# Kernel tuning notes

Hardware: AMD Instinct MI355X
Metric: run time of the kernel (lower is better)

The kernel has to match this reference:

```python
import jax, jax.numpy as jnp
import numpy as np

EMBED_DIM = 1024
NUM_HEADS = 16
HEAD_DIM = EMBED_DIM // NUM_HEADS
B, S = 2, 2048


def setup_inputs() -> dict:
    key = jax.random.key(0)
    ks = jax.random.split(key, 9)
    scale = 1.0 / np.sqrt(EMBED_DIM)
    return {
        "x": jax.random.normal(ks[0], (B, S, EMBED_DIM), dtype=jnp.float32),
        "Wq": jax.random.normal(ks[1], (EMBED_DIM, EMBED_DIM), dtype=jnp.float32) * scale,
        "bq": jnp.zeros((EMBED_DIM,), dtype=jnp.float32),
        "Wk": jax.random.normal(ks[2], (EMBED_DIM, EMBED_DIM), dtype=jnp.float32) * scale,
        "bk": jnp.zeros((EMBED_DIM,), dtype=jnp.float32),
        "Wv": jax.random.normal(ks[3], (EMBED_DIM, EMBED_DIM), dtype=jnp.float32) * scale,
        "bv": jnp.zeros((EMBED_DIM,), dtype=jnp.float32),
        "Wo": jax.random.normal(ks[4], (EMBED_DIM, EMBED_DIM), dtype=jnp.float32) * scale,
        "bo": jnp.zeros((EMBED_DIM,), dtype=jnp.float32),
    }


def _split_heads(t):
    # [B, S, E] -> [B, H, S, Dh]
    b, s, _ = t.shape
    return t.reshape(b, s, NUM_HEADS, HEAD_DIM).transpose(0, 2, 1, 3)


def reference(x, Wq, bq, Wk, bk, Wv, bv, Wo, bo):
    q = _split_heads(x @ Wq + bq)
    k = _split_heads(x @ Wk + bk)
    v = _split_heads(x @ Wv + bv)
    scale = jnp.sqrt(jnp.asarray(HEAD_DIM, dtype=x.dtype))
    scores = jnp.einsum("bhqd,bhkd->bhqk", q, k) / scale
    attn = jax.nn.softmax(scores, axis=-1)
    out = jnp.einsum("bhqk,bhkd->bhqd", attn, v)  # [B,H,S,Dh]
    out = out.transpose(0, 2, 1, 3).reshape(x.shape[0], x.shape[1], EMBED_DIM)
    return out @ Wo + bo
```

## Files before the change

### kernel.cpp

```cpp
#include <hip/hip_runtime.h>
#include <math.h>
#include <stdint.h>

typedef __bf16 bf16;
typedef __bf16 bf16x4 __attribute__((ext_vector_type(4)));
typedef __bf16 bf16x8 __attribute__((ext_vector_type(8)));
typedef float f32x4 __attribute__((ext_vector_type(4)));
typedef float f32x16 __attribute__((ext_vector_type(16)));

constexpr int E = 1024;
constexpr int S = 2048;
constexpr int H = 16;


__device__ __forceinline__ void gload16(const void* g, void* l) {
  __builtin_amdgcn_global_load_lds(
      (__attribute__((address_space(1))) void*)(uintptr_t)g,
      (__attribute__((address_space(3))) void*)(uint32_t)(uintptr_t)l, 16, 0, 0);
}

__device__ __forceinline__ f32x4 mfma16(bf16x8 a, bf16x8 b, f32x4 c) {
  return __builtin_amdgcn_mfma_f32_16x16x32_bf16(a, b, c, 0, 0, 0);
}
__device__ __forceinline__ f32x16 mfma32(bf16x8 a, bf16x8 b, f32x16 c) {
  return __builtin_amdgcn_mfma_f32_32x32x16_bf16(a, b, c, 0, 0, 0);
}

__global__ __launch_bounds__(256) void cast_x(const float* __restrict__ x,
                                              bf16* __restrict__ o) {
  const size_t i = ((size_t)blockIdx.x * 256 + threadIdx.x) * 8;
  const float4 a = *(const float4*)(x + i);
  const float4 b = *(const float4*)(x + i + 4);
  bf16x8 r;
  r[0] = (bf16)a.x; r[1] = (bf16)a.y; r[2] = (bf16)a.z; r[3] = (bf16)a.w;
  r[4] = (bf16)b.x; r[5] = (bf16)b.y; r[6] = (bf16)b.z; r[7] = (bf16)b.w;
  *(bf16x8*)(o + i) = r;
}

__global__ __launch_bounds__(256) void transpose_cast_w(
    const float* __restrict__ W0, const float* __restrict__ W1,
    const float* __restrict__ W2, const float* __restrict__ W3,
    bf16* __restrict__ T0, bf16* __restrict__ T1, bf16* __restrict__ T2,
    bf16* __restrict__ T3) {
  const float* W;
  bf16* T;
  switch (blockIdx.z) {
    case 0: W = W0; T = T0; break;
    case 1: W = W1; T = T1; break;
    case 2: W = W2; T = T2; break;
    default: W = W3; T = T3; break;
  }
  __shared__ float t[64][65];
  const int k0 = blockIdx.y * 64, n0 = blockIdx.x * 64;
  const int tr = threadIdx.x >> 4;
  const int tc = (threadIdx.x & 15) * 4;
#pragma unroll
  for (int u = 0; u < 4; ++u) {
    const float4 v = *(const float4*)(W + (size_t)(k0 + tr + u * 16) * E + n0 + tc);
    t[tr + u * 16][tc + 0] = v.x;
    t[tr + u * 16][tc + 1] = v.y;
    t[tr + u * 16][tc + 2] = v.z;
    t[tr + u * 16][tc + 3] = v.w;
  }
  __syncthreads();
#pragma unroll
  for (int u = 0; u < 4; ++u) {
    const int n = tr + u * 16;
    bf16x4 o;
#pragma unroll
    for (int i = 0; i < 4; ++i) o[i] = (bf16)t[tc + i][n];
    *(bf16x4*)(T + (size_t)(n0 + n) * E + k0 + tc) = o;
  }
}

__global__ __launch_bounds__(256) void gemm_qkv(const bf16* __restrict__ A,
                                                const bf16* __restrict__ Wt,
                                                const float* __restrict__ bq,
                                                const float* __restrict__ bk,
                                                const float* __restrict__ bv,
                                                bf16* __restrict__ qo,
                                                bf16* __restrict__ ko,
                                                bf16* __restrict__ vo) {
  __shared__ __attribute__((aligned(16))) bf16 Asm[128 * 32];
  __shared__ __attribute__((aligned(16))) bf16 Bsm[128 * 32];
  const int z = blockIdx.z;
  const bf16* Bt = Wt + (size_t)z * E * E;
  const float* bias = (z == 0) ? bq : (z == 1) ? bk : bv;
  const int tid = threadIdx.x;
  const int w = tid >> 6, lane = tid & 63, quad = lane >> 4, ln = lane & 15;
  const int bm = blockIdx.y * 128, bn = blockIdx.x * 128;
  const int wr = w >> 1, wc = w & 1;
  const int srow = w * 32 + (lane >> 2);
  const int scol = (lane & 3) * 8;
  const bf16* Ag = A + (size_t)(bm + srow) * E + scol;
  const bf16* Bg = Bt + (size_t)(bn + srow) * E + scol;
  f32x4 acc[4][4] = {};

  for (int k0 = 0; k0 < E; k0 += 32) {
    gload16(Ag + k0, &Asm[(w * 32) * 32]);
    gload16(Ag + k0 + (size_t)16 * E, &Asm[(w * 32 + 16) * 32]);
    gload16(Bg + k0, &Bsm[(w * 32) * 32]);
    gload16(Bg + k0 + (size_t)16 * E, &Bsm[(w * 32 + 16) * 32]);
    __syncthreads();
    bf16x8 af[4], bfr[4];
#pragma unroll
    for (int t = 0; t < 4; ++t) {
      af[t] = *(const bf16x8*)&Asm[(wr * 64 + t * 16 + ln) * 32 + quad * 8];
      bfr[t] = *(const bf16x8*)&Bsm[(wc * 64 + t * 16 + ln) * 32 + quad * 8];
    }
#pragma unroll
    for (int rt = 0; rt < 4; ++rt)
#pragma unroll
      for (int ct = 0; ct < 4; ++ct)
        acc[rt][ct] = mfma16(af[rt], bfr[ct], acc[rt][ct]);
    __syncthreads();
  }

  const float scl = (z == 0) ? 0.125f : 1.0f;
  const int hglob = (bn + wc * 64) >> 6;
  float bvv[4];
#pragma unroll
  for (int ct = 0; ct < 4; ++ct) bvv[ct] = bias[bn + wc * 64 + ct * 16 + ln];

#pragma unroll
  for (int rt = 0; rt < 4; ++rt) {
    const int row0 = bm + wr * 64 + rt * 16 + quad * 4;
    const int bb = row0 >> 11;
    const int rl = row0 & 2047;
    const size_t hb = (size_t)(bb * 16 + hglob) * 131072;
#pragma unroll
    for (int ct = 0; ct < 4; ++ct) {
      if (z == 2) {
        const int mt = ct >> 1, ln32 = ((ct & 1) << 4) | ln;
        const int tau = rl >> 6, hfv = (rl >> 3) & 1, j0 = rl & 7;
        bf16x4 p;
#pragma unroll
        for (int r = 0; r < 4; ++r) p[r] = (bf16)(acc[rt][ct][r] + bvv[ct]);
        *(bf16x4*)&vo[hb + (size_t)((tau * 8 + mt * 4 + rt) * 512 +
                                    hfv * 256 + ln32 * 8 + j0)] = p;
      } else {
        bf16* o = (z == 0) ? qo : ko;
        const int t = rl >> 5, ln0 = rl & 31;
        const size_t base =
            hb + (size_t)((t * 4 + ct) * 512 + (ln >> 3) * 256 + (ln & 7));
#pragma unroll
        for (int r = 0; r < 4; ++r)
          o[base + (ln0 + r) * 8] = (bf16)((acc[rt][ct][r] + bvv[ct]) * scl);
      }
    }
  }
}

__global__ __launch_bounds__(256) void gemm_wo(const bf16* __restrict__ A,
                                               const bf16* __restrict__ Bt,
                                               const float* __restrict__ bias,
                                               float* __restrict__ C) {
  __shared__ __attribute__((aligned(16))) bf16 Asm[64 * 32];
  __shared__ __attribute__((aligned(16))) bf16 Bsm[128 * 32];
  const int tid = threadIdx.x;
  const int w = tid >> 6, lane = tid & 63, quad = lane >> 4, ln = lane & 15;
  const int bm = blockIdx.y * 64, bn = blockIdx.x * 128;
  const int wr = w >> 1, wc = w & 1;
  const int sr = lane >> 2, sc = (lane & 3) * 8;
  const bf16* Ag = A + (size_t)(bm + w * 16 + sr) * E + sc;
  const bf16* Bg = Bt + (size_t)(bn + w * 32 + sr) * E + sc;
  f32x4 acc[2][4] = {};

  for (int k0 = 0; k0 < E; k0 += 32) {
    gload16(Ag + k0, &Asm[(w * 16) * 32]);
    gload16(Bg + k0, &Bsm[(w * 32) * 32]);
    gload16(Bg + k0 + (size_t)16 * E, &Bsm[(w * 32 + 16) * 32]);
    __syncthreads();
    bf16x8 af[2], bfr[4];
#pragma unroll
    for (int t = 0; t < 2; ++t)
      af[t] = *(const bf16x8*)&Asm[(wr * 32 + t * 16 + ln) * 32 + quad * 8];
#pragma unroll
    for (int t = 0; t < 4; ++t)
      bfr[t] = *(const bf16x8*)&Bsm[(wc * 64 + t * 16 + ln) * 32 + quad * 8];
#pragma unroll
    for (int rt = 0; rt < 2; ++rt)
#pragma unroll
      for (int ct = 0; ct < 4; ++ct)
        acc[rt][ct] = mfma16(af[rt], bfr[ct], acc[rt][ct]);
    __syncthreads();
  }

  float bvv[4];
#pragma unroll
  for (int ct = 0; ct < 4; ++ct) bvv[ct] = bias[bn + wc * 64 + ct * 16 + ln];
#pragma unroll
  for (int rt = 0; rt < 2; ++rt) {
    const int row0 = bm + wr * 32 + rt * 16 + quad * 4;
#pragma unroll
    for (int ct = 0; ct < 4; ++ct) {
      const int c = bn + wc * 64 + ct * 16 + ln;
#pragma unroll
      for (int r = 0; r < 4; ++r)
        C[(size_t)(row0 + r) * E + c] = acc[rt][ct][r] + bvv[ct];
    }
  }
}

__global__ __launch_bounds__(64) void attn_mfma(const bf16* __restrict__ Qf,
                                                const bf16* __restrict__ Kf,
                                                const bf16* __restrict__ Vf,
                                                bf16* __restrict__ Og) {
  __shared__ __attribute__((aligned(16))) bf16 Pl[32][74];
  const int lane = threadIdx.x;
  const int ln = lane & 31, hf = lane >> 5;
  const int tq = blockIdx.x, h = blockIdx.y, b = blockIdx.z;
  const int bh = b * H + h;
  const size_t fb = (size_t)bh * 131072;

  bf16x8 qf[4];
  {
    const bf16* qb = Qf + fb + (size_t)tq * 2048 + lane * 8;
#pragma unroll
    for (int c = 0; c < 4; ++c) qf[c] = *(const bf16x8*)(qb + c * 512);
  }

  const bf16* Kb = Kf + fb + lane * 8;
  const bf16* Vb = Vf + fb + lane * 8;

  float lpart = 0.f;
  f32x16 oacc[2] = {};

  for (int kt2 = 0; kt2 < S / 32; kt2 += 2) {
    f32x16 st[2];
#pragma unroll
    for (int mt = 0; mt < 2; ++mt) {
      const bf16* kb2 = Kb + (size_t)(kt2 + mt) * 2048;
      f32x16 zz = {};
#pragma unroll
      for (int c = 0; c < 4; ++c)
        zz = mfma32(*(const bf16x8*)(kb2 + c * 512), qf[c], zz);
      st[mt] = zz;
    }

    bf16x8 va[2][4];
    {
      const bf16* vb2 = Vb + (size_t)(kt2 >> 1) * 4096;
#pragma unroll
      for (int mt = 0; mt < 2; ++mt)
#pragma unroll
        for (int c = 0; c < 4; ++c)
          va[mt][c] = *(const bf16x8*)(vb2 + (mt * 4 + c) * 512);
    }

#pragma unroll
    for (int mt = 0; mt < 2; ++mt) {
#pragma unroll
      for (int g = 0; g < 4; ++g) {
        bf16x4 pk;
#pragma unroll
        for (int j = 0; j < 4; ++j) {
          const float p = __expf(st[mt][g * 4 + j]);
          lpart += p;
          pk[j] = (bf16)p;
        }
        *(bf16x4*)&Pl[ln][mt * 32 + g * 8 + hf * 4] = pk;
      }
    }
    asm volatile("s_waitcnt lgkmcnt(0)" ::: "memory");

    bf16x8 pb[4];
#pragma unroll
    for (int c = 0; c < 4; ++c)
      pb[c] = *(const bf16x8*)&Pl[ln][c * 16 + hf * 8];
#pragma unroll
    for (int mt = 0; mt < 2; ++mt)
#pragma unroll
      for (int c = 0; c < 4; ++c)
        oacc[mt] = mfma32(va[mt][c], pb[c], oacc[mt]);
  }

  lpart += __shfl_xor(lpart, 32);
  const float inv = 1.0f / lpart;

  bf16* orow = Og + ((size_t)b * S + (size_t)tq * 32 + ln) * E + h * 64;
#pragma unroll
  for (int mt = 0; mt < 2; ++mt) {
#pragma unroll
    for (int g = 0; g < 4; ++g) {
      bf16x4 o;
#pragma unroll
      for (int j = 0; j < 4; ++j) o[j] = (bf16)(oacc[mt][g * 4 + j] * inv);
      *(bf16x4*)&orow[mt * 32 + g * 8 + hf * 4] = o;
    }
  }
}

extern "C" void kernel_launch(void* const* d_in, const int* in_sizes, int n_in,
                              void* d_out, int out_size, void* d_ws, size_t ws_size,
                              hipStream_t stream) {
  const float* x = (const float*)d_in[0];
  const float* Wq = (const float*)d_in[1];
  const float* bq = (const float*)d_in[2];
  const float* Wk = (const float*)d_in[3];
  const float* bk = (const float*)d_in[4];
  const float* Wv = (const float*)d_in[5];
  const float* bv = (const float*)d_in[6];
  const float* Wo = (const float*)d_in[7];
  const float* bo = (const float*)d_in[8];

  const size_t ME = (size_t)4096 * 1024;
  const size_t WE = (size_t)1024 * 1024;
  bf16* xb = (bf16*)d_ws;
  bf16* wqt = xb + ME;
  bf16* wkt = wqt + WE;
  bf16* wvt = wkt + WE;
  bf16* wot = wvt + WE;
  bf16* qb = wot + WE;
  bf16* kb = qb + ME;
  bf16* vt = kb + ME;
  bf16* ab = vt + ME;

  cast_x<<<2048, 256, 0, stream>>>(x, xb);
  transpose_cast_w<<<dim3(16, 16, 4), 256, 0, stream>>>(Wq, Wk, Wv, Wo, wqt, wkt,
                                                        wvt, wot);
  gemm_qkv<<<dim3(8, 32, 3), 256, 0, stream>>>(xb, wqt, bq, bk, bv, qb, kb, vt);
  attn_mfma<<<dim3(S / 32, H, 2), 64, 0, stream>>>(qb, kb, vt, ab);
  gemm_wo<<<dim3(8, 64), 256, 0, stream>>>(ab, wot, bo, (float*)d_out);
}
```

Baseline: 204.2 us.

## Split attention keys across waves and merge partial accumulators in LDS

Attention blocks grow from one wave to four: two query tiles, each with its key range split in half across two waves. Each wave computes a partial unnormalized output and row sum. Waves with ki==1 write theirs to shared memory, and the ki==0 waves add them, normalize and store. The aim is more waves in flight and shorter per-wave serial loops, which should help latency hiding. In exchange it adds LDS traffic, a block barrier and extra LDS use. The merge is valid only because the kernel never subtracts a running max, so the partial sums combine directly.

Result: no change. 203.0 us (-0.6%).

```diff
diff --git a/kernel.cpp b/kernel.cpp
--- a/kernel.cpp
+++ b/kernel.cpp
@@ -202,16 +202,19 @@
   }
 }
 
-__global__ __launch_bounds__(64) void attn_mfma(const bf16* __restrict__ Qf,
-                                                const bf16* __restrict__ Kf,
-                                                const bf16* __restrict__ Vf,
-                                                bf16* __restrict__ Og) {
-  __shared__ __attribute__((aligned(16))) bf16 Pl[32][74];
-  const int lane = threadIdx.x;
+__global__ __launch_bounds__(256, 4) void attn_mfma(const bf16* __restrict__ Qf,
+                                                    const bf16* __restrict__ Kf,
+                                                    const bf16* __restrict__ Vf,
+                                                    bf16* __restrict__ Og) {
+  __shared__ __attribute__((aligned(16))) bf16 Pl[4][32][74];
+  __shared__ float Cb[2][32][64];
+  __shared__ float Lb[2][64];
+  const int tid = threadIdx.x;
+  const int lane = tid & 63, w = tid >> 6;
+  const int qi = w & 1, ki = w >> 1;
   const int ln = lane & 31, hf = lane >> 5;
-  const int tq = blockIdx.x, h = blockIdx.y, b = blockIdx.z;
-  const int bh = b * H + h;
-  const size_t fb = (size_t)bh * 131072;
+  const int tq = blockIdx.x * 2 + qi, h = blockIdx.y, b = blockIdx.z;
+  const size_t fb = (size_t)(b * H + h) * 131072;
 
   bf16x8 qf[4];
   {
@@ -226,7 +229,8 @@
   float lpart = 0.f;
   f32x16 oacc[2] = {};
 
-  for (int kt2 = 0; kt2 < S / 32; kt2 += 2) {
+  const int kt2lo = ki * (S / 64);
+  for (int kt2 = kt2lo; kt2 < kt2lo + S / 64; kt2 += 2) {
     f32x16 st[2];
 #pragma unroll
     for (int mt = 0; mt < 2; ++mt) {
@@ -259,7 +263,7 @@
           lpart += p;
           pk[j] = (bf16)p;
         }
-        *(bf16x4*)&Pl[ln][mt * 32 + g * 8 + hf * 4] = pk;
+        *(bf16x4*)&Pl[w][ln][mt * 32 + g * 8 + hf * 4] = pk;
       }
     }
     asm volatile("s_waitcnt lgkmcnt(0)" ::: "memory");
@@ -267,7 +271,7 @@
     bf16x8 pb[4];
 #pragma unroll
     for (int c = 0; c < 4; ++c)
-      pb[c] = *(const bf16x8*)&Pl[ln][c * 16 + hf * 8];
+      pb[c] = *(const bf16x8*)&Pl[w][ln][c * 16 + hf * 8];
 #pragma unroll
     for (int mt = 0; mt < 2; ++mt)
 #pragma unroll
@@ -275,18 +279,34 @@
         oacc[mt] = mfma32(va[mt][c], pb[c], oacc[mt]);
   }
 
-  lpart += __shfl_xor(lpart, 32);
-  const float inv = 1.0f / lpart;
-
-  bf16* orow = Og + ((size_t)b * S + (size_t)tq * 32 + ln) * E + h * 64;
-#pragma unroll
-  for (int mt = 0; mt < 2; ++mt) {
-#pragma unroll
-    for (int g = 0; g < 4; ++g) {
-      bf16x4 o;
-#pragma unroll
-      for (int j = 0; j < 4; ++j) o[j] = (bf16)(oacc[mt][g * 4 + j] * inv);
-      *(bf16x4*)&orow[mt * 32 + g * 8 + hf * 4] = o;
+  if (ki == 1) {
+#pragma unroll
+    for (int mt = 0; mt < 2; ++mt)
+#pragma unroll
+      for (int i = 0; i < 16; ++i) Cb[qi][mt * 16 + i][lane] = oacc[mt][i];
+    Lb[qi][lane] = lpart;
+  }
+  __syncthreads();
+  if (ki == 0) {
+#pragma unroll
+    for (int mt = 0; mt < 2; ++mt)
+#pragma unroll
+      for (int i = 0; i < 16; ++i) oacc[mt][i] += Cb[qi][mt * 16 + i][lane];
+    lpart += Lb[qi][lane];
+
+    lpart += __shfl_xor(lpart, 32);
+    const float inv = 1.0f / lpart;
+
+    bf16* orow = Og + ((size_t)b * S + (size_t)tq * 32 + ln) * E + h * 64;
+#pragma unroll
+    for (int mt = 0; mt < 2; ++mt) {
+#pragma unroll
+      for (int g = 0; g < 4; ++g) {
+        bf16x4 o;
+#pragma unroll
+        for (int j = 0; j < 4; ++j) o[j] = (bf16)(oacc[mt][g * 4 + j] * inv);
+        *(bf16x4*)&orow[mt * 32 + g * 8 + hf * 4] = o;
+      }
     }
   }
 }
@@ -320,6 +340,6 @@
   transpose_cast_w<<<dim3(16, 16, 4), 256, 0, stream>>>(Wq, Wk, Wv, Wo, wqt, wkt,
                                                         wvt, wot);
   gemm_qkv<<<dim3(8, 32, 3), 256, 0, stream>>>(xb, wqt, bq, bk, bv, qb, kb, vt);
-  attn_mfma<<<dim3(S / 32, H, 2), 64, 0, stream>>>(qb, kb, vt, ab);
+  attn_mfma<<<dim3(S / 64, H, 2), 256, 0, stream>>>(qb, kb, vt, ab);
   gemm_wo<<<dim3(8, 64), 256, 0, stream>>>(ab, wot, bo, (float*)d_out);
 }
```

## Share K/V tiles in LDS across query waves and split keys between wave groups

Applied to the files above, without the earlier changes.

The attention kernel becomes a 512-thread block of 8 waves. Four query tiles share K/V tiles that are loaded into LDS with global_load_lds, instead of each 64-thread block reading K/V straight from global memory. The key range is split between two wave groups, and their partial outputs and row sums are combined through LDS at the end. This aims to cut redundant global K/V traffic and raise reuse, at the cost of block-level barriers every iteration, no double-buffering, and an extra combine step.

New measurement: 191.5 us. 1.07x faster.

```diff
diff --git a/kernel.cpp b/kernel.cpp
--- a/kernel.cpp
+++ b/kernel.cpp
@@ -24,6 +24,9 @@
 }
 __device__ __forceinline__ f32x16 mfma32(bf16x8 a, bf16x8 b, f32x16 c) {
   return __builtin_amdgcn_mfma_f32_32x32x16_bf16(a, b, c, 0, 0, 0);
+}
+__device__ __forceinline__ void lgkm0() {
+  asm volatile("s_waitcnt lgkmcnt(0)" ::: "memory");
 }
 
 __global__ __launch_bounds__(256) void cast_x(const float* __restrict__ x,
@@ -202,16 +205,21 @@
   }
 }
 
-__global__ __launch_bounds__(64) void attn_mfma(const bf16* __restrict__ Qf,
-                                                const bf16* __restrict__ Kf,
-                                                const bf16* __restrict__ Vf,
-                                                bf16* __restrict__ Og) {
-  __shared__ __attribute__((aligned(16))) bf16 Pl[32][74];
-  const int lane = threadIdx.x;
-  const int ln = lane & 31, hf = lane >> 5;
-  const int tq = blockIdx.x, h = blockIdx.y, b = blockIdx.z;
-  const int bh = b * H + h;
-  const size_t fb = (size_t)bh * 131072;
+__global__ __launch_bounds__(512, 4) void attn_mfma(const bf16* __restrict__ Qf,
+                                                    const bf16* __restrict__ Kf,
+                                                    const bf16* __restrict__ Vf,
+                                                    bf16* __restrict__ Og) {
+  __shared__ __attribute__((aligned(16))) char smem[49152];
+  bf16* KsB = (bf16*)smem;
+  bf16* VsB = (bf16*)(smem + 16384);
+  bf16* PlB = (bf16*)(smem + 32768);
+
+  const int tid = threadIdx.x;
+  const int w = tid >> 6, lane = tid & 63, ln = lane & 31, hf = lane >> 5;
+  const int qi = w & 3, ki = w >> 2;
+  const int tq = blockIdx.x * 4 + qi;
+  const int h = blockIdx.y, b = blockIdx.z;
+  const size_t fb = (size_t)(b * H + h) * 131072;
 
   bf16x8 qf[4];
   {
@@ -220,73 +228,95 @@
     for (int c = 0; c < 4; ++c) qf[c] = *(const bf16x8*)(qb + c * 512);
   }
 
-  const bf16* Kb = Kf + fb + lane * 8;
-  const bf16* Vb = Vf + fb + lane * 8;
+  bf16* Ks = KsB + ki * 4096;
+  bf16* Vs = VsB + ki * 4096;
+  bf16* Pw = PlB + w * 1024;
+
+  const bf16* Ksrc = Kf + fb + qi * 1024 + lane * 8;
+  const bf16* Vsrc = Vf + fb + qi * 1024 + lane * 8;
+  bf16* Kdst = Ks + qi * 1024;
+  bf16* Vdst = Vs + qi * 1024;
 
   float lpart = 0.f;
   f32x16 oacc[2] = {};
 
-  for (int kt2 = 0; kt2 < S / 32; kt2 += 2) {
-    f32x16 st[2];
+  for (int i = 0; i < 16; ++i) {
+    const size_t toff = (size_t)(ki * 16 + i) * 4096;
+    gload16(Ksrc + toff, Kdst);
+    gload16(Ksrc + toff + 512, Kdst + 512);
+    gload16(Vsrc + toff, Vdst);
+    gload16(Vsrc + toff + 512, Vdst + 512);
+    __syncthreads();
+
 #pragma unroll
     for (int mt = 0; mt < 2; ++mt) {
-      const bf16* kb2 = Kb + (size_t)(kt2 + mt) * 2048;
-      f32x16 zz = {};
+      f32x16 st = {};
 #pragma unroll
       for (int c = 0; c < 4; ++c)
-        zz = mfma32(*(const bf16x8*)(kb2 + c * 512), qf[c], zz);
-      st[mt] = zz;
-    }
-
-    bf16x8 va[2][4];
-    {
-      const bf16* vb2 = Vb + (size_t)(kt2 >> 1) * 4096;
-#pragma unroll
-      for (int mt = 0; mt < 2; ++mt)
-#pragma unroll
-        for (int c = 0; c < 4; ++c)
-          va[mt][c] = *(const bf16x8*)(vb2 + (mt * 4 + c) * 512);
-    }
-
-#pragma unroll
-    for (int mt = 0; mt < 2; ++mt) {
+        st = mfma32(*(const bf16x8*)&Ks[(mt * 4 + c) * 512 + lane * 8], qf[c], st);
+
 #pragma unroll
       for (int g = 0; g < 4; ++g) {
         bf16x4 pk;
 #pragma unroll
         for (int j = 0; j < 4; ++j) {
-          const float p = __expf(st[mt][g * 4 + j]);
+          const float p = __expf(st[g * 4 + j]);
           lpart += p;
           pk[j] = (bf16)p;
         }
-        *(bf16x4*)&Pl[ln][mt * 32 + g * 8 + hf * 4] = pk;
+        *(bf16x4*)&Pw[g * 256 + ln * 8 + hf * 4] = pk;
       }
-    }
-    asm volatile("s_waitcnt lgkmcnt(0)" ::: "memory");
-
-    bf16x8 pb[4];
-#pragma unroll
-    for (int c = 0; c < 4; ++c)
-      pb[c] = *(const bf16x8*)&Pl[ln][c * 16 + hf * 8];
-#pragma unroll
-    for (int mt = 0; mt < 2; ++mt)
-#pragma unroll
-      for (int c = 0; c < 4; ++c)
-        oacc[mt] = mfma32(va[mt][c], pb[c], oacc[mt]);
-  }
-
-  lpart += __shfl_xor(lpart, 32);
-  const float inv = 1.0f / lpart;
-
-  bf16* orow = Og + ((size_t)b * S + (size_t)tq * 32 + ln) * E + h * 64;
-#pragma unroll
-  for (int mt = 0; mt < 2; ++mt) {
-#pragma unroll
-    for (int g = 0; g < 4; ++g) {
-      bf16x4 o;
-#pragma unroll
-      for (int j = 0; j < 4; ++j) o[j] = (bf16)(oacc[mt][g * 4 + j] * inv);
-      *(bf16x4*)&orow[mt * 32 + g * 8 + hf * 4] = o;
+      lgkm0();
+
+      const bf16x8 pb0 = *(const bf16x8*)&Pw[lane * 8];
+      const bf16x8 pb1 = *(const bf16x8*)&Pw[512 + lane * 8];
+      lgkm0();
+
+#pragma unroll
+      for (int vt = 0; vt < 2; ++vt) {
+        oacc[vt] = mfma32(
+            *(const bf16x8*)&Vs[(vt * 4 + mt * 2 + 0) * 512 + lane * 8], pb0,
+            oacc[vt]);
+        oacc[vt] = mfma32(
+            *(const bf16x8*)&Vs[(vt * 4 + mt * 2 + 1) * 512 + lane * 8], pb1,
+            oacc[vt]);
+      }
+    }
+    __syncthreads();
+  }
+
+  float* Ocmb = (float*)smem;
+  float* Lcmb = (float*)(smem + 32768);
+  if (ki == 1) {
+#pragma unroll
+    for (int vt = 0; vt < 2; ++vt)
+#pragma unroll
+      for (int r = 0; r < 16; ++r)
+        Ocmb[qi * 2048 + (vt * 16 + r) * 64 + lane] = oacc[vt][r];
+    Lcmb[qi * 64 + lane] = lpart;
+  }
+  __syncthreads();
+  if (ki == 0) {
+#pragma unroll
+    for (int vt = 0; vt < 2; ++vt)
+#pragma unroll
+      for (int r = 0; r < 16; ++r)
+        oacc[vt][r] += Ocmb[qi * 2048 + (vt * 16 + r) * 64 + lane];
+    lpart += Lcmb[qi * 64 + lane];
+
+    lpart += __shfl_xor(lpart, 32);
+    const float inv = 1.0f / lpart;
+
+    bf16* orow = Og + ((size_t)b * S + (size_t)tq * 32 + ln) * E + h * 64;
+#pragma unroll
+    for (int vt = 0; vt < 2; ++vt) {
+#pragma unroll
+      for (int g = 0; g < 4; ++g) {
+        bf16x4 o;
+#pragma unroll
+        for (int j = 0; j < 4; ++j) o[j] = (bf16)(oacc[vt][g * 4 + j] * inv);
+        *(bf16x4*)&orow[vt * 32 + g * 8 + hf * 4] = o;
+      }
     }
   }
 }
@@ -320,6 +350,6 @@
   transpose_cast_w<<<dim3(16, 16, 4), 256, 0, stream>>>(Wq, Wk, Wv, Wo, wqt, wkt,
                                                         wvt, wot);
   gemm_qkv<<<dim3(8, 32, 3), 256, 0, stream>>>(xb, wqt, bq, bk, bv, qb, kb, vt);
-  attn_mfma<<<dim3(S / 32, H, 2), 64, 0, stream>>>(qb, kb, vt, ab);
+  attn_mfma<<<dim3(S / 128, H, 2), 512, 0, stream>>>(qb, kb, vt, ab);
   gemm_wo<<<dim3(8, 64), 256, 0, stream>>>(ab, wot, bo, (float*)d_out);
 }
```
